# Performance work log

Hardware: AMD Instinct MI355X
Metric: run time of the kernel (lower is better)

Reference implementation:

```python
import jax, jax.numpy as jnp
import numpy as np

B, H, W, C = 4, 128, 128, 256
SHIFTS_LOCAL = (1, 2, 4, 8)
SHIFTS_GLOBAL = (1, 2)
LN_EPS = 1e-6
BN_EPS = 1e-3
LAYER_SCALE_INIT = 1e-5


def _glorot(key, shape, fan_in, fan_out):
    lim = (6.0 / (fan_in + fan_out)) ** 0.5
    return jax.random.uniform(key, shape, minval=-lim, maxval=lim, dtype=jnp.float32)


def setup_inputs() -> dict:
    key = jax.random.key(0)
    ks = jax.random.split(key, 10)
    x = jax.random.normal(ks[0], (B, H, W, C), jnp.float32)
    ln_gamma = jnp.ones((C,), jnp.float32)
    w_det = _glorot(ks[1], (C, C), C, C)
    dw1 = _glorot(ks[2], (3, 3, 1, C), 9, 9)   # depthwise 3x3, HWIO with I=1
    dw2 = _glorot(ks[3], (3, 3, 1, C), 9, 9)
    bn_gamma = jnp.ones((C,), jnp.float32)
    bn_mean = jax.random.normal(ks[4], (C,), jnp.float32) * 0.1
    bn_var = jax.random.uniform(ks[5], (C,), minval=0.5, maxval=1.5, dtype=jnp.float32)
    n_loc = 2 * len(SHIFTS_LOCAL) * C   # 'full' mode: sym + antisym per shift
    n_glo = 2 * len(SHIFTS_GLOBAL) * C
    w_geo_local = _glorot(ks[6], (n_loc, C), n_loc, C)
    w_geo_global = _glorot(ks[7], (n_glo, C), n_glo, C)
    w_gate = _glorot(ks[8], (2 * C, C), 2 * C, C)
    gamma_ls = jnp.full((C,), LAYER_SCALE_INIT, jnp.float32)
    return {
        "x": x, "ln_gamma": ln_gamma, "w_det": w_det, "dw1": dw1, "dw2": dw2,
        "bn_gamma": bn_gamma, "bn_mean": bn_mean, "bn_var": bn_var,
        "w_geo_local": w_geo_local, "w_geo_global": w_geo_global,
        "w_gate": w_gate, "gamma_ls": gamma_ls,
    }


def _dwconv(x, k):
    # depthwise 3x3 same conv, NHWC, kernel HWIO with I=1, groups=C
    return jax.lax.conv_general_dilated(
        x, k, window_strides=(1, 1), padding='SAME',
        dimension_numbers=('NHWC', 'HWIO', 'NHWC'),
        feature_group_count=x.shape[-1])


def _geo_prod(a, b, shifts, w):
    # sparse rolling geometric product, cli_mode='full': for each channel
    # shift s emit symmetric (inner) and antisymmetric (wedge) parts, then
    # project the concat back to C channels (bias-free Dense).
    feats = []
    for s in shifts:
        b_s = jnp.roll(b, s, axis=-1)
        a_s = jnp.roll(a, s, axis=-1)
        feats.append(a * b_s + a_s * b)   # inner (symmetric)
        feats.append(a * b_s - a_s * b)   # wedge (antisymmetric)
    return jnp.concatenate(feats, axis=-1) @ w


def reference(x, ln_gamma, w_det, dw1, dw2, bn_gamma, bn_mean, bn_var,
              w_geo_local, w_geo_global, w_gate, gamma_ls):
    # LayerNorm, center=False (scale-only, mean still subtracted)
    mu = jnp.mean(x, axis=-1, keepdims=True)
    var = jnp.var(x, axis=-1, keepdims=True)
    x_norm = (x - mu) / jnp.sqrt(var + LN_EPS) * ln_gamma
    # deterministic stream: bias-free Dense
    z_det = x_norm @ w_det
    # context stream: two depthwise convs + scale-only BN (inference) + SiLU
    z_ctx = _dwconv(_dwconv(x_norm, dw1), dw2)
    z_ctx = jax.nn.silu((z_ctx - bn_mean) / jnp.sqrt(bn_var + BN_EPS) * bn_gamma)
    # ctx_mode='diff'
    z_ctx = z_ctx - z_det
    g_feat = _geo_prod(z_det, z_ctx, SHIFTS_LOCAL, w_geo_local)
    # global context branch
    c_glo = jnp.mean(x_norm, axis=(1, 2), keepdims=True) - z_det
    g_feat = g_feat + _geo_prod(z_det, c_glo, SHIFTS_GLOBAL, w_geo_global)
    # bias-free gated geometric residual (drop_path_rate=0 => identity)
    alpha = jax.nn.sigmoid(jnp.concatenate([x_norm, g_feat], axis=-1) @ w_gate)
    h_mix = (jax.nn.silu(x_norm) + alpha * g_feat) * gamma_ls
    return x + h_mix
```

## Files before the change

kernel.cpp:

```cpp
#include <hip/hip_runtime.h>

typedef __attribute__((ext_vector_type(8))) short bf16x8;
typedef __attribute__((ext_vector_type(8))) unsigned short ushort8;
typedef __attribute__((ext_vector_type(4))) unsigned short ushort4v;
typedef __attribute__((ext_vector_type(4))) float f32x4;
typedef __attribute__((ext_vector_type(8))) _Float16 f16x8;

__device__ inline unsigned short f2bf(float f){
  unsigned u = __builtin_bit_cast(unsigned, f);
  return (unsigned short)((u + 0x7fffu + ((u>>16)&1u)) >> 16);
}
__device__ inline float bf2f(unsigned short h){
  return __builtin_bit_cast(float, (unsigned)h << 16);
}
__device__ inline unsigned short f2h(float f){
  return __builtin_bit_cast(unsigned short, (_Float16)f);
}
__device__ inline float h2f(unsigned short u){
  return (float)__builtin_bit_cast(_Float16, u);
}

__device__ inline void gll16(const void* g, void* l){
  __builtin_amdgcn_global_load_lds((const __attribute__((address_space(1))) void*)g,
                                   (__attribute__((address_space(3))) void*)l, 16, 0, 0);
}

__global__ __launch_bounds__(256) void k_ln(const float* __restrict__ x,
                                            const float* __restrict__ g,
                                            unsigned short* __restrict__ A3){
  int r = blockIdx.x, c = threadIdx.x;
  float v = x[(size_t)r*256 + c];
  float s = v, s2 = v*v;
  #pragma unroll
  for (int m=32; m>=1; m>>=1){ s += __shfl_xor(s, m, 64); s2 += __shfl_xor(s2, m, 64); }
  __shared__ float rs[4], rs2[4];
  int wid = c>>6, lane = c&63;
  if (lane==0){ rs[wid]=s; rs2[wid]=s2; }
  __syncthreads();
  float ts  = rs[0]+rs[1]+rs[2]+rs[3];
  float ts2 = rs2[0]+rs2[1]+rs2[2]+rs2[3];
  float mu  = ts*(1.f/256.f);
  float var = ts2*(1.f/256.f) - mu*mu;
  float xn = (v-mu)*rsqrtf(var + 1e-6f)*g[c];
  A3[(size_t)r*512 + c] = f2bf(xn);
}

__global__ __launch_bounds__(256) void k_cm1(const unsigned short* __restrict__ A3,
                                             float* __restrict__ psum){
  int blk = blockIdx.x;
  int c = threadIdx.x;
  const unsigned short* base = A3 + (size_t)blk*256*512;
  float s = 0.f;
  for (int p=0;p<256;p++) s += bf2f(base[(size_t)p*512 + c]);
  psum[blk*256 + c] = s;
}
__global__ __launch_bounds__(256) void k_cm2(const float* __restrict__ psum,
                                             float* __restrict__ m){
  int b = blockIdx.x, c = threadIdx.x;
  float s = 0.f;
  for (int ch=0; ch<64; ch++) s += psum[(b*64+ch)*256 + c];
  m[b*256 + c] = s*(1.f/16384.f);
}

__global__ __launch_bounds__(256) void k_prep_nt(const float* __restrict__ W,
                                                 unsigned short* __restrict__ WT, int K){
  int idx = blockIdx.x*256 + threadIdx.x;
  int j = idx / K, k = idx - j*K;
  WT[idx] = f2bf(W[(size_t)k*256 + j]);
}

__global__ __launch_bounds__(256) void k_prep_geoT(const float* __restrict__ wl,
                                                   const float* __restrict__ wg,
                                                   unsigned short* __restrict__ WT){
  int idx = blockIdx.x*256 + threadIdx.x;
  int e = idx & 7, n = (idx>>3)&255, q = (idx>>11)&3, k32 = (idx>>13)&7, sg = idx>>16;
  int k = k32*32 + q*8 + e;
  int j = n;
  float v;
  if (sg < 8){
    int si = sg >> 1, s = 1 << si;
    bool neg = sg & 1;
    int krow = neg ? ((k + s) & 255) : k;
    float wi = wl[(size_t)((2*si)*256 + krow)*256 + j];
    float ww = wl[(size_t)((2*si+1)*256 + krow)*256 + j];
    v = neg ? (wi - ww) : (wi + ww);
  } else {
    v = -2.f * wg[(size_t)((sg-8)*2*256 + k)*256 + j];
  }
  WT[idx] = f2h(v);
}

__global__ __launch_bounds__(256) void k_prep_weff(const float* __restrict__ wg,
                                                   const float* __restrict__ m,
                                                   unsigned short* __restrict__ WT){
  int b = blockIdx.x >> 8, c = blockIdx.x & 255, j = threadIdx.x;
  float acc = 0.f;
  #pragma unroll
  for (int si=0; si<2; ++si){
    int s = si+1;
    int cm = (c - s) & 255, cp = (c + s) & 255;
    float wi_c  = wg[(size_t)((2*si)*256 + c)*256 + j];
    float ww_c  = wg[(size_t)((2*si+1)*256 + c)*256 + j];
    float wi_cp = wg[(size_t)((2*si)*256 + cp)*256 + j];
    float ww_cp = wg[(size_t)((2*si+1)*256 + cp)*256 + j];
    acc += m[b*256+cm]*(wi_c+ww_c) + m[b*256+cp]*(wi_cp-ww_cp);
  }
  size_t addr = (size_t)b*65536 + (size_t)(c>>5)*8192 + (size_t)((c>>3)&3)*2048
              + (size_t)j*8 + (c&7);
  WT[addr] = f2h(acc);
}

__global__ __launch_bounds__(256) void k_dwf(const unsigned short* __restrict__ A3,
                                             const float* __restrict__ w1g,
                                             const float* __restrict__ w2g,
                                             const float* __restrict__ bg,
                                             const float* __restrict__ bm_,
                                             const float* __restrict__ bv,
                                             const unsigned short* __restrict__ zdet,
                                             unsigned short* __restrict__ zcx){
  __shared__ unsigned short t0[12800];
  __shared__ unsigned short t1[10368];
  int t = blockIdx.x;
  int img = t >> 6, ty = (t>>3)&7, tx = t&7;
  int c0 = blockIdx.y*32;
  int tid = threadIdx.x;
  int ch = tid & 31;
  int c = c0 + ch;
  for (int v = tid; v < 3200; v += 256){
    int py = v / 160, rem = v - py*160;
    int px = rem >> 3, ch4 = (rem & 7)*4;
    int gpy = ty*16 - 2 + py, gpx = tx*16 - 2 + px;
    ushort4v val = {0,0,0,0};
    if ((unsigned)gpy < 128u && (unsigned)gpx < 128u){
      size_t gp = (size_t)(img*16384 + gpy*128 + gpx);
      val = *(const ushort4v*)&A3[gp*512 + c0 + ch4];
    }
    *(ushort4v*)&t0[(py*20+px)*32 + ch4] = val;
  }
  float w1[9], w2[9];
  #pragma unroll
  for (int k=0;k<9;k++){ w1[k] = w1g[k*256 + c]; w2[k] = w2g[k*256 + c]; }
  __syncthreads();
  for (int p = tid>>5; p < 324; p += 8){
    int py = p / 18, px = p - py*18;
    int gpy = ty*16 - 1 + py, gpx = tx*16 - 1 + px;
    float acc = 0.f;
    #pragma unroll
    for (int dy=0; dy<3; ++dy)
      #pragma unroll
      for (int dx=0; dx<3; ++dx)
        acc += bf2f(t0[((py+dy)*20 + px+dx)*32 + ch]) * w1[dy*3+dx];
    bool valid = ((unsigned)gpy < 128u) && ((unsigned)gpx < 128u);
    t1[p*32 + ch] = valid ? f2h(acc) : (unsigned short)0;
  }
  __syncthreads();
  float bmv = bm_[c];
  float rsbg = rsqrtf(bv[c] + 1e-3f) * bg[c];
  for (int p = tid>>5; p < 256; p += 8){
    int py = p >> 4, px = p & 15;
    float acc = 0.f;
    #pragma unroll
    for (int dy=0; dy<3; ++dy)
      #pragma unroll
      for (int dx=0; dx<3; ++dx)
        acc += h2f(t1[((py+dy)*18 + px+dx)*32 + ch]) * w2[dy*3+dx];
    float tv = (acc - bmv) * rsbg;
    float sv = tv / (1.f + __expf(-tv));
    size_t gp = (size_t)(img*16384 + (ty*16+py)*128 + tx*16+px);
    float z = sv - h2f(zdet[gp*256 + c]);
    zcx[gp*256 + c] = f2h(z);
  }
}

template<int EPI>
__global__ __launch_bounds__(256) void k_gemm(const unsigned short* __restrict__ A, int lda,
                                              const unsigned short* __restrict__ Bt, int K,
                                              unsigned short* __restrict__ outh,
                                              const float* __restrict__ xin,
                                              const unsigned short* __restrict__ A3,
                                              const float* __restrict__ gls,
                                              float* __restrict__ out){
  __shared__ unsigned short As[128*64];
  __shared__ unsigned short Bs[128*64];
  const int tid=threadIdx.x, lane=tid&63, wid=tid>>6;
  const int bm = blockIdx.x*128, bn = blockIdx.y*128;
  const int wr = wid>>1, wc = wid&1;
  f32x4 acc[4][4] = {};
  const int nk = K>>6;
  const int srow = lane>>3;
  const int skc  = ((lane&7) ^ srow) * 8;
  for (int t=0; t<nk; ++t){
    int k0 = t*64;
    #pragma unroll
    for (int i=0;i<4;i++){
      int q = wid*4 + i;
      int row = q*8 + srow;
      gll16(A  + (size_t)(bm+row)*lda + k0 + skc, &As[q*512]);
      gll16(Bt + (size_t)(bn+row)*K   + k0 + skc, &Bs[q*512]);
    }
    __syncthreads();
    #pragma unroll
    for (int kk=0; kk<2; ++kk){
      bf16x8 af[4], bfr[4];
      #pragma unroll
      for (int i=0;i<4;i++){
        int rl = wr*64 + i*16 + (lane&15);
        int kc = (kk*32 + (lane>>4)*8) ^ ((rl&7)*8);
        af[i]  = *(const bf16x8*)&As[rl*64 + kc];
        int cl = wc*64 + i*16 + (lane&15);
        int kcb = (kk*32 + (lane>>4)*8) ^ ((cl&7)*8);
        bfr[i] = *(const bf16x8*)&Bs[cl*64 + kcb];
      }
      #pragma unroll
      for (int i=0;i<4;i++)
        #pragma unroll
        for (int j=0;j<4;j++)
          acc[i][j] = __builtin_amdgcn_mfma_f32_16x16x32_bf16(af[i], bfr[j], acc[i][j], 0,0,0);
    }
    __syncthreads();
  }
  #pragma unroll
  for (int i=0;i<4;i++)
    #pragma unroll
    for (int j=0;j<4;j++)
      #pragma unroll
      for (int r=0;r<4;r++){
        int row = bm + wr*64 + i*16 + (lane>>4)*4 + r;
        int col = bn + wc*64 + j*16 + (lane&15);
        float v = acc[i][j][r];
        if constexpr (EPI==0){
          outh[(size_t)row*256 + col] = f2h(v);
        } else {
          float alpha = 1.f/(1.f+__expf(-v));
          float xnv = bf2f(A3[(size_t)row*512 + col]);
          float gfv = bf2f(A3[(size_t)row*512 + 256 + col]);
          float sl = xnv/(1.f+__expf(-xnv));
          out[(size_t)row*256 + col] = xin[(size_t)row*256 + col] + (sl + alpha*gfv)*gls[col];
        }
      }
}

template<int S>
__device__ __attribute__((always_inline)) ushort8 shsel(ushort8 hi, ushort8 lo){
  ushort8 r;
  if constexpr (S==0) return hi;
  #pragma unroll
  for (int e=0;e<8;e++) r[e] = (e<S) ? lo[8-S+e] : hi[e-S];
  return r;
}

template<int SEG>
__device__ __attribute__((always_inline)) f16x8 gen2(ushort8 zdh, ushort8 zdl,
      ushort8 zch, ushort8 zcl, ushort8 zcu){
  if constexpr (SEG==10) return __builtin_bit_cast(f16x8, zdh);
  ushort8 sel;
  if constexpr      (SEG==0) sel = shsel<1>(zch, zcl);
  else if constexpr (SEG==1) sel = shsel<7>(zcu, zch);
  else if constexpr (SEG==2) sel = shsel<2>(zch, zcl);
  else if constexpr (SEG==3) sel = shsel<6>(zcu, zch);
  else if constexpr (SEG==4) sel = shsel<4>(zch, zcl);
  else if constexpr (SEG==5) sel = shsel<4>(zcu, zch);
  else if constexpr (SEG==6) sel = zcl;
  else if constexpr (SEG==7) sel = zcu;
  else if constexpr (SEG==8) sel = shsel<1>(zdh, zdl);
  else                       sel = shsel<2>(zdh, zdl);
  return __builtin_bit_cast(f16x8, zdh) * __builtin_bit_cast(f16x8, sel);
}

__global__ __launch_bounds__(256, 2) void k_geo(const unsigned short* __restrict__ zd,
                                                const unsigned short* __restrict__ zc,
                                                const unsigned short* __restrict__ WT_all,
                                                const unsigned short* __restrict__ WeffT,
                                                unsigned short* __restrict__ A3){
  __shared__ unsigned short Bs[4][8192];
  const int tid = threadIdx.x, lane = tid&63, wid = tid>>6;
  const int bm = blockIdx.x*64;
  const int img = blockIdx.x >> 8;
  f32x4 acc[4][4] = {};

  int boff[4];
  #pragma unroll
  for (int fj=0; fj<4; ++fj){
    int n = wid*64 + fj*16 + (lane&15);
    boff[fj] = (lane>>4)*2048 + n*8;
  }

  const int mrow = bm + (lane&15);
  const unsigned short* zr[4];
  const unsigned short* cr[4];
  #pragma unroll
  for (int rg=0; rg<4; ++rg){
    zr[rg] = zd + (size_t)(mrow + rg*16)*256;
    cr[rg] = zc + (size_t)(mrow + rg*16)*256;
  }

  ushort8 zdh[4], zdl[4], zch[4], zcl[4], zcu[4];
  int cur = 0;

#define STAGE(BUF, SP, KK) { \
    const unsigned short* src = (((SP)<10) ? (WT_all + (size_t)(SP)*65536) \
                                           : (WeffT + (size_t)img*65536)) \
                                + (size_t)(KK)*8192 + wid*2048 + lane*8; \
    gll16(src,        &Bs[BUF][wid*2048]); \
    gll16(src + 512,  &Bs[BUF][wid*2048 + 512]); \
    gll16(src + 1024, &Bs[BUF][wid*2048 + 1024]); \
    gll16(src + 1536, &Bs[BUF][wid*2048 + 1536]); \
  }

  STAGE(0, 0, 0)
  STAGE(1, 1, 0)
  STAGE(2, 2, 0)

#define STEP(P) { \
    if constexpr ((P)==1 || (P)==2){ asm volatile("s_waitcnt vmcnt(28)" ::: "memory"); } \
    else                           { asm volatile("s_waitcnt vmcnt(8)"  ::: "memory"); } \
    __builtin_amdgcn_s_barrier(); \
    if constexpr ((P)==0){ \
      int kc = k32*32 + (lane>>4)*8; \
      int kl = (kc-8)&255, ku = (kc+8)&255; \
      _Pragma("unroll") \
      for (int rg=0; rg<4; ++rg){ \
        zdh[rg] = *(const ushort8*)(zr[rg] + kc); \
        zdl[rg] = *(const ushort8*)(zr[rg] + kl); \
        zch[rg] = *(const ushort8*)(cr[rg] + kc); \
        zcl[rg] = *(const ushort8*)(cr[rg] + kl); \
        zcu[rg] = *(const ushort8*)(cr[rg] + ku); \
      } \
      __builtin_amdgcn_sched_barrier(0); \
    } \
    { constexpr int s3 = ((P)+3)%11; \
      int k3 = k32 + (((P)>=8) ? 1 : 0); if (k3 > 7) k3 = 7; \
      STAGE((cur+3)&3, s3, k3) } \
    f16x8 af[4]; \
    _Pragma("unroll") \
    for (int rg=0; rg<4; ++rg) af[rg] = gen2<(P)>(zdh[rg],zdl[rg],zch[rg],zcl[rg],zcu[rg]); \
    const unsigned short* bp = &Bs[cur][0]; \
    __builtin_amdgcn_s_setprio(1); \
    _Pragma("unroll") \
    for (int fj=0; fj<4; ++fj){ \
      f16x8 bfr = *(const f16x8*)&bp[boff[fj]]; \
      _Pragma("unroll") \
      for (int rg=0; rg<4; ++rg) \
        acc[rg][fj] = __builtin_amdgcn_mfma_f32_16x16x32_f16(af[rg], bfr, acc[rg][fj], 0,0,0); \
    } \
    __builtin_amdgcn_s_setprio(0); \
    cur = (cur+1)&3; \
  }

  for (int k32=0; k32<8; ++k32){
    STEP(0) STEP(1) STEP(2) STEP(3) STEP(4) STEP(5)
    STEP(6) STEP(7) STEP(8) STEP(9) STEP(10)
  }
#undef STEP
#undef STAGE

  #pragma unroll
  for (int rg=0; rg<4; ++rg)
    #pragma unroll
    for (int fj=0; fj<4; ++fj)
      #pragma unroll
      for (int r=0; r<4; ++r){
        int row = bm + rg*16 + (lane>>4)*4 + r;
        int col = wid*64 + fj*16 + (lane&15);
        A3[(size_t)row*512 + 256 + col] = f2bf(acc[rg][fj][r]);
      }
}

extern "C" void kernel_launch(void* const* d_in, const int* in_sizes, int n_in,
                              void* d_out, int out_size, void* d_ws, size_t ws_size,
                              hipStream_t stream){
  (void)in_sizes; (void)n_in; (void)out_size; (void)ws_size;
  const float* x    = (const float*)d_in[0];
  const float* lng  = (const float*)d_in[1];
  const float* wdet = (const float*)d_in[2];
  const float* dw1  = (const float*)d_in[3];
  const float* dw2  = (const float*)d_in[4];
  const float* bng  = (const float*)d_in[5];
  const float* bnm  = (const float*)d_in[6];
  const float* bnv  = (const float*)d_in[7];
  const float* wloc = (const float*)d_in[8];
  const float* wglo = (const float*)d_in[9];
  const float* wgat = (const float*)d_in[10];
  const float* gls  = (const float*)d_in[11];
  float* out = (float*)d_out;
  char* ws = (char*)d_ws;

  unsigned short* A3     = (unsigned short*)(ws);
  unsigned short* ZDET   = (unsigned short*)(ws + 67108864);
  unsigned short* ZCX    = (unsigned short*)(ws + 134217728);
  unsigned short* WTALL  = (unsigned short*)(ws + 167772160);
  unsigned short* WEFFT  = (unsigned short*)(ws + 169213952);
  unsigned short* WDETT  = (unsigned short*)(ws + 169738240);
  unsigned short* WGATET = (unsigned short*)(ws + 169869312);
  float* PSUM  = (float*)(ws + 170131456);
  float* MMEAN = (float*)(ws + 170393600);

  k_ln<<<65536, 256, 0, stream>>>(x, lng, A3);
  k_cm1<<<256, 256, 0, stream>>>(A3, PSUM);
  k_cm2<<<4, 256, 0, stream>>>(PSUM, MMEAN);
  k_prep_nt<<<256, 256, 0, stream>>>(wdet, WDETT, 256);
  k_prep_nt<<<512, 256, 0, stream>>>(wgat, WGATET, 512);
  k_prep_geoT<<<2560, 256, 0, stream>>>(wloc, wglo, WTALL);
  k_prep_weff<<<1024, 256, 0, stream>>>(wglo, MMEAN, WEFFT);
  k_gemm<0><<<dim3(512,2), 256, 0, stream>>>(A3, 512, WDETT, 256, ZDET,
                                             nullptr, nullptr, nullptr, nullptr);
  k_dwf<<<dim3(256,8), 256, 0, stream>>>(A3, dw1, dw2, bng, bnm, bnv, ZDET, ZCX);
  k_geo<<<1024, 256, 0, stream>>>(ZDET, ZCX, WTALL, WEFFT, A3);
  k_gemm<1><<<dim3(512,2), 256, 0, stream>>>(A3, 512, WGATET, 512, nullptr,
                                             x, A3, gls, out);
}
```

Baseline: 354.6 us.

## Load B fragments directly into registers with double-buffered prefetch, drop LDS staging

The geo GEMM kernel no longer stages weight tiles in shared memory through global_load_lds with barriers. Each wave now loads its MFMA B fragments straight from global memory into registers, using a two-deep register double buffer that prefetches two segments ahead. The A-side operand loads are spread across segments 8 and 10 of the previous k-step instead of happening all at once. This removes LDS traffic and block barriers, at the cost of more VGPRs and possibly less coalesced global loads, and it exposes global latency.

Measured after the change: 360.5 us. About the same (+1.7%).

```diff
diff --git a/kernel.cpp b/kernel.cpp
--- a/kernel.cpp
+++ b/kernel.cpp
@@ -5,6 +5,7 @@
 typedef __attribute__((ext_vector_type(4))) unsigned short ushort4v;
 typedef __attribute__((ext_vector_type(4))) float f32x4;
 typedef __attribute__((ext_vector_type(8))) _Float16 f16x8;
+typedef __attribute__((ext_vector_type(4))) unsigned uint4v;
 
 __device__ inline unsigned short f2bf(float f){
   unsigned u = __builtin_bit_cast(unsigned, f);
@@ -272,18 +273,12 @@
                                                 const unsigned short* __restrict__ WT_all,
                                                 const unsigned short* __restrict__ WeffT,
                                                 unsigned short* __restrict__ A3){
-  __shared__ unsigned short Bs[4][8192];
   const int tid = threadIdx.x, lane = tid&63, wid = tid>>6;
   const int bm = blockIdx.x*64;
-  const int img = blockIdx.x >> 8;
+  const size_t weffoff = (size_t)(blockIdx.x >> 8)*65536;
   f32x4 acc[4][4] = {};
 
-  int boff[4];
-  #pragma unroll
-  for (int fj=0; fj<4; ++fj){
-    int n = wid*64 + fj*16 + (lane&15);
-    boff[fj] = (lane>>4)*2048 + n*8;
-  }
+  const size_t fragoff = (size_t)(lane>>4)*2048 + (size_t)(wid*64 + (lane&15))*8;
 
   const int mrow = bm + (lane&15);
   const unsigned short* zr[4];
@@ -295,64 +290,94 @@
   }
 
   ushort8 zdh[4], zdl[4], zch[4], zcl[4], zcu[4];
-  int cur = 0;
-
-#define STAGE(BUF, SP, KK) { \
-    const unsigned short* src = (((SP)<10) ? (WT_all + (size_t)(SP)*65536) \
-                                           : (WeffT + (size_t)img*65536)) \
-                                + (size_t)(KK)*8192 + wid*2048 + lane*8; \
-    gll16(src,        &Bs[BUF][wid*2048]); \
-    gll16(src + 512,  &Bs[BUF][wid*2048 + 512]); \
-    gll16(src + 1024, &Bs[BUF][wid*2048 + 1024]); \
-    gll16(src + 1536, &Bs[BUF][wid*2048 + 1536]); \
-  }
-
-  STAGE(0, 0, 0)
-  STAGE(1, 1, 0)
-  STAGE(2, 2, 0)
-
-#define STEP(P) { \
-    if constexpr ((P)==1 || (P)==2){ asm volatile("s_waitcnt vmcnt(28)" ::: "memory"); } \
-    else                           { asm volatile("s_waitcnt vmcnt(8)"  ::: "memory"); } \
-    __builtin_amdgcn_s_barrier(); \
-    if constexpr ((P)==0){ \
-      int kc = k32*32 + (lane>>4)*8; \
-      int kl = (kc-8)&255, ku = (kc+8)&255; \
+  uint4v fb[2][4];
+
+  {
+    int kc = (lane>>4)*8, kl = (kc-8)&255, ku = (kc+8)&255;
+    #pragma unroll
+    for (int rg=0; rg<4; ++rg){
+      zdh[rg] = *(const ushort8*)(zr[rg] + kc);
+      zdl[rg] = *(const ushort8*)(zr[rg] + kl);
+      zch[rg] = *(const ushort8*)(cr[rg] + kc);
+      zcl[rg] = *(const ushort8*)(cr[rg] + kl);
+      zcu[rg] = *(const ushort8*)(cr[rg] + ku);
+    }
+    const unsigned short* p0 = WT_all + fragoff;
+    const unsigned short* p1 = WT_all + 65536 + fragoff;
+    #pragma unroll
+    for (int f=0; f<4; ++f){
+      fb[0][f] = *(const uint4v*)(p0 + f*128);
+      fb[1][f] = *(const uint4v*)(p1 + f*128);
+    }
+  }
+
+#define FRAG_PREFETCH(SEG, B) { \
+    constexpr int sg2 = ((SEG)+2)%11; \
+    int k32p = k32 + (((SEG)>=9)?1:0); if (k32p>7) k32p=7; \
+    const unsigned short* p2 = ((sg2<10)? (WT_all + (size_t)sg2*65536) \
+                                        : (WeffT + weffoff)) \
+                               + (size_t)k32p*8192 + fragoff; \
+    fb[B][0] = *(const uint4v*)(p2); \
+    fb[B][1] = *(const uint4v*)(p2+128); \
+    fb[B][2] = *(const uint4v*)(p2+256); \
+    fb[B][3] = *(const uint4v*)(p2+384); \
+  }
+
+#define STEPX(SEG, B) { \
+    f16x8 bfr[4]; \
+    bfr[0] = __builtin_bit_cast(f16x8, fb[B][0]); \
+    bfr[1] = __builtin_bit_cast(f16x8, fb[B][1]); \
+    bfr[2] = __builtin_bit_cast(f16x8, fb[B][2]); \
+    bfr[3] = __builtin_bit_cast(f16x8, fb[B][3]); \
+    FRAG_PREFETCH(SEG, B) \
+    if constexpr ((SEG)==8){ \
+      int k32n = (k32<7)? k32+1 : 7; \
+      int kc2 = k32n*32 + (lane>>4)*8; \
+      int kl2 = (kc2-8)&255, ku2 = (kc2+8)&255; \
       _Pragma("unroll") \
       for (int rg=0; rg<4; ++rg){ \
-        zdh[rg] = *(const ushort8*)(zr[rg] + kc); \
-        zdl[rg] = *(const ushort8*)(zr[rg] + kl); \
-        zch[rg] = *(const ushort8*)(cr[rg] + kc); \
-        zcl[rg] = *(const ushort8*)(cr[rg] + kl); \
-        zcu[rg] = *(const ushort8*)(cr[rg] + ku); \
+        zch[rg] = *(const ushort8*)(cr[rg] + kc2); \
+        zcl[rg] = *(const ushort8*)(cr[rg] + kl2); \
+        zcu[rg] = *(const ushort8*)(cr[rg] + ku2); \
       } \
-      __builtin_amdgcn_sched_barrier(0); \
     } \
-    { constexpr int s3 = ((P)+3)%11; \
-      int k3 = k32 + (((P)>=8) ? 1 : 0); if (k3 > 7) k3 = 7; \
-      STAGE((cur+3)&3, s3, k3) } \
     f16x8 af[4]; \
     _Pragma("unroll") \
-    for (int rg=0; rg<4; ++rg) af[rg] = gen2<(P)>(zdh[rg],zdl[rg],zch[rg],zcl[rg],zcu[rg]); \
-    const unsigned short* bp = &Bs[cur][0]; \
+    for (int rg=0; rg<4; ++rg) af[rg] = gen2<(SEG)>(zdh[rg],zdl[rg],zch[rg],zcl[rg],zcu[rg]); \
+    if constexpr ((SEG)==10){ \
+      int k32n = (k32<7)? k32+1 : 7; \
+      int kc2 = k32n*32 + (lane>>4)*8; \
+      int kl2 = (kc2-8)&255; \
+      _Pragma("unroll") \
+      for (int rg=0; rg<4; ++rg){ \
+        zdh[rg] = *(const ushort8*)(zr[rg] + kc2); \
+        zdl[rg] = *(const ushort8*)(zr[rg] + kl2); \
+      } \
+    } \
     __builtin_amdgcn_s_setprio(1); \
     _Pragma("unroll") \
     for (int fj=0; fj<4; ++fj){ \
-      f16x8 bfr = *(const f16x8*)&bp[boff[fj]]; \
       _Pragma("unroll") \
       for (int rg=0; rg<4; ++rg) \
-        acc[rg][fj] = __builtin_amdgcn_mfma_f32_16x16x32_f16(af[rg], bfr, acc[rg][fj], 0,0,0); \
+        acc[rg][fj] = __builtin_amdgcn_mfma_f32_16x16x32_f16(af[rg], bfr[fj], acc[rg][fj], 0,0,0); \
     } \
     __builtin_amdgcn_s_setprio(0); \
-    cur = (cur+1)&3; \
-  }
-
-  for (int k32=0; k32<8; ++k32){
-    STEP(0) STEP(1) STEP(2) STEP(3) STEP(4) STEP(5)
-    STEP(6) STEP(7) STEP(8) STEP(9) STEP(10)
-  }
-#undef STEP
-#undef STAGE
+  }
+
+  for (int k2=0; k2<4; ++k2){
+    {
+      int k32 = 2*k2;
+      STEPX(0,0) STEPX(1,1) STEPX(2,0) STEPX(3,1) STEPX(4,0) STEPX(5,1)
+      STEPX(6,0) STEPX(7,1) STEPX(8,0) STEPX(9,1) STEPX(10,0)
+    }
+    {
+      int k32 = 2*k2+1;
+      STEPX(0,1) STEPX(1,0) STEPX(2,1) STEPX(3,0) STEPX(4,1) STEPX(5,0)
+      STEPX(6,1) STEPX(7,0) STEPX(8,1) STEPX(9,0) STEPX(10,1)
+    }
+  }
+#undef STEPX
+#undef FRAG_PREFETCH
 
   #pragma unroll
   for (int rg=0; rg<4; ++rg)
```

## Warp-specialize geo GEMM with dedicated producer wave and 128-row tiles

Applied to the files above, without the earlier changes.

Restructures k_geo so that a ninth wavefront acts only as a producer, streaming weight tiles into the 4-deep LDS ring via global_load_lds. The eight consumer waves do only the MFMA work. The block tile grows to 128 rows across 8 compute waves (2 row halves x 4 column quarters), which halves how many times each block restreams the weights. Activation loads are double-buffered in registers so the next k-slice is prefetched one step ahead. The risks are lower occupancy (576 threads, no min-blocks hint), the correctness of the barrier/vmcnt handshake between producer and consumers, and register pressure from the duplicated operand buffers.

New measurement: 538.8 us. 1.52x slower.

```diff
diff --git a/kernel.cpp b/kernel.cpp
--- a/kernel.cpp
+++ b/kernel.cpp
@@ -267,92 +267,115 @@
   return __builtin_bit_cast(f16x8, zdh) * __builtin_bit_cast(f16x8, sel);
 }
 
-__global__ __launch_bounds__(256, 2) void k_geo(const unsigned short* __restrict__ zd,
-                                                const unsigned short* __restrict__ zc,
-                                                const unsigned short* __restrict__ WT_all,
-                                                const unsigned short* __restrict__ WeffT,
-                                                unsigned short* __restrict__ A3){
+__global__ __launch_bounds__(576) void k_geo(const unsigned short* __restrict__ zd,
+                                             const unsigned short* __restrict__ zc,
+                                             const unsigned short* __restrict__ WT_all,
+                                             const unsigned short* __restrict__ WeffT,
+                                             unsigned short* __restrict__ A3){
   __shared__ unsigned short Bs[4][8192];
   const int tid = threadIdx.x, lane = tid&63, wid = tid>>6;
-  const int bm = blockIdx.x*64;
-  const int img = blockIdx.x >> 8;
+  const int bm = blockIdx.x*128;
+  const int img = blockIdx.x >> 7;
+  const unsigned short* weff = WeffT + (size_t)img*65536;
+
+  if (wid == 8){
+    unsigned short* lds0 = &Bs[0][0];
+    #pragma unroll
+    for (int s=0; s<3; ++s){
+      const unsigned short* src = WT_all + (size_t)s*65536 + lane*8;
+      unsigned short* dst = lds0 + s*8192 + lane*8;
+      #pragma unroll
+      for (int g=0; g<16; ++g) gll16(src + g*512, dst + g*512);
+    }
+    for (int t=0; t<88; ++t){
+      asm volatile("s_waitcnt vmcnt(32)" ::: "memory");
+      __builtin_amdgcn_s_barrier();
+      int st = t+3; if (st > 87) st = 87;
+      int k32 = (st*373)>>12;
+      int seg = st - k32*11;
+      const unsigned short* src = ((seg<10) ? (WT_all + (size_t)seg*65536) : weff)
+                                  + (size_t)k32*8192 + lane*8;
+      unsigned short* dst = lds0 + ((t+3)&3)*8192 + lane*8;
+      #pragma unroll
+      for (int g=0; g<16; ++g) gll16(src + g*512, dst + g*512);
+    }
+    return;
+  }
+
+  const int cq = wid & 3, rh = wid >> 2;
   f32x4 acc[4][4] = {};
-
-  int boff[4];
-  #pragma unroll
-  for (int fj=0; fj<4; ++fj){
-    int n = wid*64 + fj*16 + (lane&15);
-    boff[fj] = (lane>>4)*2048 + n*8;
-  }
-
-  const int mrow = bm + (lane&15);
-  const unsigned short* zr[4];
-  const unsigned short* cr[4];
+  const int boff = (lane>>4)*2048 + (cq*64 + (lane&15))*8;
+  const unsigned short* ldsF = &Bs[0][0];
+  int curh = 0;
+
+  const int mrow = bm + rh*64 + (lane&15);
+  const unsigned short* zrow[4];
+  const unsigned short* crow[4];
   #pragma unroll
   for (int rg=0; rg<4; ++rg){
-    zr[rg] = zd + (size_t)(mrow + rg*16)*256;
-    cr[rg] = zc + (size_t)(mrow + rg*16)*256;
-  }
-
-  ushort8 zdh[4], zdl[4], zch[4], zcl[4], zcu[4];
-  int cur = 0;
-
-#define STAGE(BUF, SP, KK) { \
-    const unsigned short* src = (((SP)<10) ? (WT_all + (size_t)(SP)*65536) \
-                                           : (WeffT + (size_t)img*65536)) \
-                                + (size_t)(KK)*8192 + wid*2048 + lane*8; \
-    gll16(src,        &Bs[BUF][wid*2048]); \
-    gll16(src + 512,  &Bs[BUF][wid*2048 + 512]); \
-    gll16(src + 1024, &Bs[BUF][wid*2048 + 1024]); \
-    gll16(src + 1536, &Bs[BUF][wid*2048 + 1536]); \
-  }
-
-  STAGE(0, 0, 0)
-  STAGE(1, 1, 0)
-  STAGE(2, 2, 0)
-
-#define STEP(P) { \
-    if constexpr ((P)==1 || (P)==2){ asm volatile("s_waitcnt vmcnt(28)" ::: "memory"); } \
-    else                           { asm volatile("s_waitcnt vmcnt(8)"  ::: "memory"); } \
+    zrow[rg] = zd + (size_t)(mrow + rg*16)*256;
+    crow[rg] = zc + (size_t)(mrow + rg*16)*256;
+  }
+
+  ushort8 zdhA[4], zdlA[4], zchA[4], zclA[4], zcuA[4];
+  ushort8 zdhB[4], zdlB[4], zchB[4], zclB[4], zcuB[4];
+
+#define LOAD_OPS(BK, K32) { \
+    int kc_ = (K32)*32 + (lane>>4)*8; \
+    int kl_ = (kc_-8)&255, ku_ = (kc_+8)&255; \
+    _Pragma("unroll") \
+    for (int rg=0; rg<4; ++rg){ \
+      zdh##BK[rg] = *(const ushort8*)(zrow[rg] + kc_); \
+      zdl##BK[rg] = *(const ushort8*)(zrow[rg] + kl_); \
+      zch##BK[rg] = *(const ushort8*)(crow[rg] + kc_); \
+      zcl##BK[rg] = *(const ushort8*)(crow[rg] + kl_); \
+      zcu##BK[rg] = *(const ushort8*)(crow[rg] + ku_); \
+    } }
+
+#define CSTEP(SEG, BK, PF) { \
     __builtin_amdgcn_s_barrier(); \
-    if constexpr ((P)==0){ \
-      int kc = k32*32 + (lane>>4)*8; \
-      int kl = (kc-8)&255, ku = (kc+8)&255; \
-      _Pragma("unroll") \
-      for (int rg=0; rg<4; ++rg){ \
-        zdh[rg] = *(const ushort8*)(zr[rg] + kc); \
-        zdl[rg] = *(const ushort8*)(zr[rg] + kl); \
-        zch[rg] = *(const ushort8*)(cr[rg] + kc); \
-        zcl[rg] = *(const ushort8*)(cr[rg] + kl); \
-        zcu[rg] = *(const ushort8*)(cr[rg] + ku); \
-      } \
-      __builtin_amdgcn_sched_barrier(0); \
-    } \
-    { constexpr int s3 = ((P)+3)%11; \
-      int k3 = k32 + (((P)>=8) ? 1 : 0); if (k3 > 7) k3 = 7; \
-      STAGE((cur+3)&3, s3, k3) } \
+    __builtin_amdgcn_sched_barrier(0); \
+    PF \
+    f16x8 bfr[4]; \
+    const unsigned short* bp = ldsF + curh + boff; \
+    bfr[0] = *(const f16x8*)(bp); \
+    bfr[1] = *(const f16x8*)(bp + 128); \
+    bfr[2] = *(const f16x8*)(bp + 256); \
+    bfr[3] = *(const f16x8*)(bp + 384); \
     f16x8 af[4]; \
     _Pragma("unroll") \
-    for (int rg=0; rg<4; ++rg) af[rg] = gen2<(P)>(zdh[rg],zdl[rg],zch[rg],zcl[rg],zcu[rg]); \
-    const unsigned short* bp = &Bs[cur][0]; \
+    for (int rg=0; rg<4; ++rg) \
+      af[rg] = gen2<(SEG)>(zdh##BK[rg],zdl##BK[rg],zch##BK[rg],zcl##BK[rg],zcu##BK[rg]); \
     __builtin_amdgcn_s_setprio(1); \
     _Pragma("unroll") \
     for (int fj=0; fj<4; ++fj){ \
-      f16x8 bfr = *(const f16x8*)&bp[boff[fj]]; \
       _Pragma("unroll") \
       for (int rg=0; rg<4; ++rg) \
-        acc[rg][fj] = __builtin_amdgcn_mfma_f32_16x16x32_f16(af[rg], bfr, acc[rg][fj], 0,0,0); \
+        acc[rg][fj] = __builtin_amdgcn_mfma_f32_16x16x32_f16(af[rg], bfr[fj], acc[rg][fj], 0,0,0); \
     } \
     __builtin_amdgcn_s_setprio(0); \
-    cur = (cur+1)&3; \
-  }
-
-  for (int k32=0; k32<8; ++k32){
-    STEP(0) STEP(1) STEP(2) STEP(3) STEP(4) STEP(5)
-    STEP(6) STEP(7) STEP(8) STEP(9) STEP(10)
-  }
-#undef STEP
-#undef STAGE
+    curh = (curh + 8192) & 32767; \
+  }
+
+#define ROUND(K32, BK, NBK) \
+    CSTEP(0, BK, ) \
+    CSTEP(1, BK, LOAD_OPS(NBK, ((K32)<7 ? (K32)+1 : 7))) \
+    CSTEP(2, BK, ) CSTEP(3, BK, ) CSTEP(4, BK, ) CSTEP(5, BK, ) \
+    CSTEP(6, BK, ) CSTEP(7, BK, ) CSTEP(8, BK, ) CSTEP(9, BK, ) \
+    CSTEP(10, BK, )
+
+  LOAD_OPS(A, 0)
+  ROUND(0, A, B)
+  ROUND(1, B, A)
+  ROUND(2, A, B)
+  ROUND(3, B, A)
+  ROUND(4, A, B)
+  ROUND(5, B, A)
+  ROUND(6, A, B)
+  ROUND(7, B, A)
+#undef ROUND
+#undef CSTEP
+#undef LOAD_OPS
 
   #pragma unroll
   for (int rg=0; rg<4; ++rg)
@@ -360,8 +383,8 @@
     for (int fj=0; fj<4; ++fj)
       #pragma unroll
       for (int r=0; r<4; ++r){
-        int row = bm + rg*16 + (lane>>4)*4 + r;
-        int col = wid*64 + fj*16 + (lane&15);
+        int row = bm + rh*64 + rg*16 + (lane>>4)*4 + r;
+        int col = cq*64 + fj*16 + (lane&15);
         A3[(size_t)row*512 + 256 + col] = f2bf(acc[rg][fj][r]);
       }
 }
@@ -405,7 +428,7 @@
   k_gemm<0><<<dim3(512,2), 256, 0, stream>>>(A3, 512, WDETT, 256, ZDET,
                                              nullptr, nullptr, nullptr, nullptr);
   k_dwf<<<dim3(256,8), 256, 0, stream>>>(A3, dw1, dw2, bng, bnm, bnv, ZDET, ZCX);
-  k_geo<<<1024, 256, 0, stream>>>(ZDET, ZCX, WTALL, WEFFT, A3);
+  k_geo<<<512, 576, 0, stream>>>(ZDET, ZCX, WTALL, WEFFT, A3);
   k_gemm<1><<<dim3(512,2), 256, 0, stream>>>(A3, 512, WGATET, 512, nullptr,
                                              x, A3, gls, out);
 }
```
